# Optimization experiments

Hardware: AMD Instinct MI355X
Metric: run time of the kernel (lower is better)

The kernel has to match this reference:

```python
import jax, jax.numpy as jnp
import numpy as np

EPS = 1e-5  # norm_eps


def setup_inputs() -> dict:
    key = jax.random.key(0)
    ks = jax.random.split(key, 9)
    N, C, T, H, W = 2, 1024, 8, 28, 28
    Di = 512
    s = 0.02  # weight init scale
    return {
        "x": jax.random.normal(ks[0], (N, C, T, H, W), jnp.float32),
        "w_theta": jax.random.normal(ks[1], (Di, C), jnp.float32) * s,
        "b_theta": jax.random.normal(ks[2], (Di,), jnp.float32) * s,
        "w_phi": jax.random.normal(ks[3], (Di, C), jnp.float32) * s,
        "b_phi": jax.random.normal(ks[4], (Di,), jnp.float32) * s,
        "w_g": jax.random.normal(ks[5], (Di, C), jnp.float32) * s,
        "b_g": jax.random.normal(ks[6], (Di,), jnp.float32) * s,
        "w_out": jax.random.normal(ks[7], (C, Di), jnp.float32) * s,
        "b_out": jax.random.normal(ks[8], (C,), jnp.float32) * s,
    }


def reference(x, w_theta, b_theta, w_phi, b_phi, w_g, b_g, w_out, b_out):
    # ProgressNL forward at step==0 (y == x), pool_size=None,
    # instantiation='softmax', norm_type='layernorm' (GroupNorm(1, C, affine=False)).
    N, C, T, H, W = x.shape
    Di = w_theta.shape[0]
    xf = x.reshape(N, C, T * H * W)  # flatten spatio-temporal tokens

    # 1x1x1 convs == per-token matmuls
    theta = jnp.einsum('dc,nct->ndt', w_theta, xf) + b_theta[None, :, None]  # [N,Di,THW]
    phi = jnp.einsum('dc,nct->ndt', w_phi, xf) + b_phi[None, :, None]
    g = jnp.einsum('dc,nct->ndt', w_g, xf) + b_g[None, :, None]

    # attention: softmax(theta^T phi / sqrt(Di)) @ g^T
    scores = jnp.einsum('nct,ncp->ntp', theta, phi) * (Di ** -0.5)  # [N,THW,THW]
    attn = jax.nn.softmax(scores, axis=-1)
    o = jnp.einsum('ntp,ncp->nct', attn, g)  # [N,Di,THW]

    # output 1x1x1 conv
    p = jnp.einsum('cd,ndt->nct', w_out, o) + b_out[None, :, None]  # [N,C,THW]

    # GroupNorm(1, C, affine=False): normalize over (C,T,H,W) per sample
    mean = jnp.mean(p, axis=(1, 2), keepdims=True)
    var = jnp.var(p, axis=(1, 2), keepdims=True)
    p = (p - mean) * jax.lax.rsqrt(var + EPS)

    return x + p.reshape(N, C, T, H, W)
```

## Files before the change

kernel.cpp:

```cpp
#include <hip/hip_runtime.h>

typedef _Float16 f16x8 __attribute__((ext_vector_type(8)));
typedef _Float16 f16x4 __attribute__((ext_vector_type(4)));
typedef float    f32x4 __attribute__((ext_vector_type(4)));

#define THW 6272
#define CCH 1024
#define DI  512

__device__ __forceinline__ void gload16(const _Float16* g, _Float16* l)
{
    __builtin_amdgcn_global_load_lds(
        (const __attribute__((address_space(1))) void*)g,
        (__attribute__((address_space(3))) void*)l, 16, 0, 0);
}

template<typename OUT_T, int BM, bool BIAS_M, bool BIAS_N, bool EXPP>
__global__ __launch_bounds__(256, 3)
void gemm_nt(const _Float16* __restrict__ A, size_t lda, size_t sAn,
             const _Float16* __restrict__ Bt, size_t ldb, size_t sBn,
             OUT_T* __restrict__ C, size_t ldc, size_t sCn,
             int K, float alpha,
             const float* __restrict__ bias_m,
             const float* __restrict__ bias_n,
             float* __restrict__ psum,
             int rows_ps,
             int gx, int gy)
{
    constexpr int MF = BM / 32;
    __shared__ _Float16 As[BM * 64];
    __shared__ _Float16 Bs[128 * 64];
    const int tid  = threadIdx.x;
    const int lane = tid & 63;
    const int wave = tid >> 6;
    const int wr = wave >> 1, wc = wave & 1;

    const int nwg = gridDim.x;
    const int q = nwg >> 3, rr = nwg & 7;
    const int xcd = blockIdx.x & 7, seq = blockIdx.x >> 3;
    const int wg = (xcd < rr ? xcd * (q + 1) : rr * (q + 1) + (xcd - rr) * q) + seq;
    const int zz  = wg / (gx * gy);
    const int rem = wg - zz * gx * gy;
    const int by  = rem / gx, bx = rem - by * gx;
    const int n   = zz & 1;
    const int ks  = zz >> 1;

    A  += (size_t)n * sAn + (size_t)ks * K + (size_t)by * BM * lda;
    Bt += (size_t)n * sBn + (size_t)ks * K + (size_t)bx * 128 * ldb;

    const int srow = lane >> 3, sk = (lane & 7) * 8;
    const _Float16* gA = A  + (size_t)(wave * (MF * 8) + srow) * lda + sk;
    const _Float16* gB = Bt + (size_t)(wave * 32 + srow) * ldb + sk;
    _Float16* lA = As + wave * (MF * 512) + lane * 8;
    _Float16* lB = Bs + wave * 2048 + lane * 8;

    const int r  = lane & 15;
    const int kg = lane >> 4;

    f32x4 acc[MF][4] = {};

    for (int kt = 0; kt < K; kt += 64) {
#pragma unroll
        for (int i = 0; i < MF; i++)
            gload16(gA + (size_t)(i * 8) * lda, lA + i * 512);
#pragma unroll
        for (int i = 0; i < 4; i++)
            gload16(gB + (size_t)(i * 8) * ldb, lB + i * 512);
        gA += 64; gB += 64;
        __syncthreads();
#pragma unroll
        for (int kk = 0; kk < 2; kk++) {
            f16x8 af[MF], bf[4];
#pragma unroll
            for (int mf = 0; mf < MF; mf++)
                af[mf] = *(const f16x8*)(As + (wr * (BM / 2) + mf * 16 + r) * 64 + kk * 32 + kg * 8);
#pragma unroll
            for (int nf = 0; nf < 4; nf++)
                bf[nf] = *(const f16x8*)(Bs + (wc * 64 + nf * 16 + r) * 64 + kk * 32 + kg * 8);
#pragma unroll
            for (int mf = 0; mf < MF; mf++)
#pragma unroll
                for (int nf = 0; nf < 4; nf++)
                    acc[mf][nf] = __builtin_amdgcn_mfma_f32_16x16x32_f16(
                        af[mf], bf[nf], acc[mf][nf], 0, 0, 0);
        }
        __syncthreads();
    }

    C += (size_t)zz * sCn;
#pragma unroll
    for (int mf = 0; mf < MF; mf++) {
#pragma unroll
        for (int qi = 0; qi < 4; qi++) {
            size_t row = (size_t)by * BM + wr * (BM / 2) + mf * 16 + kg * 4 + qi;
            float bm = BIAS_M ? bias_m[row] : 0.f;
            float rsum = 0.f;
#pragma unroll
            for (int nf = 0; nf < 4; nf++) {
                size_t col = (size_t)bx * 128 + wc * 64 + nf * 16 + r;
                float val = acc[mf][nf][qi] * alpha + bm + (BIAS_N ? bias_n[col] : 0.f);
                if (EXPP) {
                    float e = __expf(val);
                    rsum += e;
                    C[row * ldc + col] = (OUT_T)e;
                } else {
                    C[row * ldc + col] = (OUT_T)val;
                }
            }
            if (EXPP) {
                rsum += __shfl_xor(rsum, 1);
                rsum += __shfl_xor(rsum, 2);
                rsum += __shfl_xor(rsum, 4);
                rsum += __shfl_xor(rsum, 8);
                if (r == 0)
                    psum[((size_t)n * rows_ps + row) * 98 + bx * 2 + wc] = rsum;
            }
        }
    }
}

__global__ __launch_bounds__(256)
void rowsum_inv(const float* __restrict__ psum, float* __restrict__ inv, int nrows)
{
    int rI = blockIdx.x * 256 + threadIdx.x;
    if (rI < nrows) {
        const float* p = psum + (size_t)rI * 98;
        float s = 0.f;
#pragma unroll 7
        for (int i = 0; i < 98; i++) s += p[i];
        inv[rI] = 1.f / s;
    }
}

__global__ __launch_bounds__(256)
void combine_scale(const float* __restrict__ Op, const float* __restrict__ inv,
                   _Float16* __restrict__ Ot, int tr, int t0)
{
    const int total4 = tr * 256;
    int idx = blockIdx.x * 256 + threadIdx.x;
    if (idx >= total4) return;
    const int per_n4 = tr * 128;
    int n = idx / per_n4;
    int rem = idx - n * per_n4;
    int t = rem >> 7, d4 = rem & 127;
    const f32x4* p = (const f32x4*)Op;
    f32x4 a = p[(size_t)n * per_n4 + rem];
    f32x4 b = p[(size_t)(2 + n) * per_n4 + rem];
    float sc = inv[(size_t)n * tr + t];
    f16x4 o;
#pragma unroll
    for (int j = 0; j < 4; j++) o[j] = (_Float16)((a[j] + b[j]) * sc);
    *(f16x4*)(Ot + ((size_t)(n * THW + t0 + t) * DI + d4 * 4)) = o;
}

__global__ __launch_bounds__(256)
void pack_weights(const float* __restrict__ wt, const float* __restrict__ wp,
                  const float* __restrict__ wg, const float* __restrict__ wo,
                  const float* __restrict__ bt, const float* __restrict__ bp,
                  _Float16* __restrict__ Wtp, _Float16* __restrict__ Wg,
                  _Float16* __restrict__ Wo, float* __restrict__ btp)
{
    int i = blockIdx.x * 256 + threadIdx.x;
    if (i < 512 * 1024) {
        Wtp[i]              = (_Float16)wt[i];
        Wtp[i + 512 * 1024] = (_Float16)wp[i];
        Wg[i]               = (_Float16)wg[i];
        Wo[i]               = (_Float16)wo[i];
    }
    if (i < 512) { btp[i] = bt[i]; btp[i + 512] = bp[i]; }
}

__global__ __launch_bounds__(256)
void transpose_cast(const float* __restrict__ x, _Float16* __restrict__ xT)
{
    __shared__ float tile[32][33];
    const int n  = blockIdx.z;
    const int t0 = blockIdx.x * 32;
    const int c0 = blockIdx.y * 32;
    const int tx = threadIdx.x & 31, ty = threadIdx.x >> 5;
    const float* xp = x + ((size_t)n * CCH + c0) * THW + t0;
#pragma unroll
    for (int i = 0; i < 4; i++) {
        int c = ty + i * 8;
        tile[c][tx] = xp[(size_t)c * THW + tx];
    }
    __syncthreads();
    _Float16* op = xT + ((size_t)n * THW + t0) * CCH + c0;
#pragma unroll
    for (int i = 0; i < 4; i++) {
        int t = ty + i * 8;
        op[(size_t)t * CCH + tx] = (_Float16)tile[tx][t];
    }
}

__global__ __launch_bounds__(256)
void reduce_partial(const float* __restrict__ pc, float* __restrict__ partials, int nblk)
{
    const size_t per_n4 = (size_t)CCH * THW / 4;
    const int n = blockIdx.y;
    const f32x4* p = (const f32x4*)(pc + (size_t)n * CCH * THW);
    float s = 0.f, s2 = 0.f;
    for (size_t i = (size_t)blockIdx.x * 256 + threadIdx.x; i < per_n4; i += (size_t)nblk * 256) {
        f32x4 xv = p[i];
#pragma unroll
        for (int j = 0; j < 4; j++) { s += xv[j]; s2 += xv[j] * xv[j]; }
    }
    for (int o = 32; o; o >>= 1) { s += __shfl_xor(s, o); s2 += __shfl_xor(s2, o); }
    __shared__ float rs[4], rs2[4];
    if ((threadIdx.x & 63) == 0) { rs[threadIdx.x >> 6] = s; rs2[threadIdx.x >> 6] = s2; }
    __syncthreads();
    if (threadIdx.x == 0) {
        partials[((size_t)n * nblk + blockIdx.x) * 2]     = rs[0] + rs[1] + rs[2] + rs[3];
        partials[((size_t)n * nblk + blockIdx.x) * 2 + 1] = rs2[0] + rs2[1] + rs2[2] + rs2[3];
    }
}

__global__ __launch_bounds__(256)
void reduce_final(const float* __restrict__ partials, float* __restrict__ stats, int nblk)
{
    const int n = blockIdx.x;
    float s = 0.f, s2 = 0.f;
    for (int i = threadIdx.x; i < nblk; i += 256) {
        s  += partials[((size_t)n * nblk + i) * 2];
        s2 += partials[((size_t)n * nblk + i) * 2 + 1];
    }
    for (int o = 32; o; o >>= 1) { s += __shfl_xor(s, o); s2 += __shfl_xor(s2, o); }
    __shared__ float rs[4], rs2[4];
    if ((threadIdx.x & 63) == 0) { rs[threadIdx.x >> 6] = s; rs2[threadIdx.x >> 6] = s2; }
    __syncthreads();
    if (threadIdx.x == 0) {
        float S1 = rs[0] + rs[1] + rs[2] + rs[3];
        float S2 = rs2[0] + rs2[1] + rs2[2] + rs2[3];
        const float invc = 1.f / ((float)CCH * (float)THW);
        float mean = S1 * invc;
        float var  = S2 * invc - mean * mean;
        stats[n * 2]     = mean;
        stats[n * 2 + 1] = rsqrtf(var + 1e-5f);
    }
}

__global__ __launch_bounds__(256)
void final_residual(const float* __restrict__ x, float* __restrict__ pc_out,
                    const float* __restrict__ stats, size_t total4)
{
    const size_t per_n4 = (size_t)CCH * THW / 4;
    for (size_t i = (size_t)blockIdx.x * 256 + threadIdx.x; i < total4;
         i += (size_t)gridDim.x * 256) {
        int n = (int)(i / per_n4);
        float mean = stats[n * 2], rstd = stats[n * 2 + 1];
        f32x4 xv = ((const f32x4*)x)[i];
        f32x4 pv = ((f32x4*)pc_out)[i];
        f32x4 ov;
#pragma unroll
        for (int j = 0; j < 4; j++) ov[j] = xv[j] + (pv[j] - mean) * rstd;
        ((f32x4*)pc_out)[i] = ov;
    }
}

extern "C" void kernel_launch(void* const* d_in, const int* in_sizes, int n_in,
                              void* d_out, int out_size, void* d_ws, size_t ws_size,
                              hipStream_t stream)
{
    const float* x  = (const float*)d_in[0];
    const float* wt = (const float*)d_in[1];
    const float* bt = (const float*)d_in[2];
    const float* wp = (const float*)d_in[3];
    const float* bp = (const float*)d_in[4];
    const float* wg = (const float*)d_in[5];
    const float* bg = (const float*)d_in[6];
    const float* wo = (const float*)d_in[7];
    const float* bo = (const float*)d_in[8];
    float* out = (float*)d_out;

    char* ws = (char*)d_ws;
    size_t off = 0;
    auto alloc = [&](size_t b) -> void* {
        off = (off + 255) & ~(size_t)255;
        void* p = ws + off;
        off += b;
        return p;
    };

    _Float16* Wtp = (_Float16*)alloc((size_t)1024 * 1024 * 2);
    _Float16* Wg  = (_Float16*)alloc((size_t)512 * 1024 * 2);
    _Float16* Wo  = (_Float16*)alloc((size_t)1024 * 512 * 2);
    float*    btp = (float*)alloc(1024 * 4);
    _Float16* xT  = (_Float16*)alloc((size_t)2 * THW * CCH * 2);
    _Float16* tpg = (_Float16*)alloc((size_t)2 * THW * 1024 * 2);
    _Float16* g   = (_Float16*)alloc((size_t)2 * DI * THW * 2);
    _Float16* Ot  = (_Float16*)alloc((size_t)2 * THW * DI * 2);
    float*    partials = (float*)alloc((size_t)2 * 256 * 2 * 4);
    float*    stats    = (float*)alloc(4 * 4);

    const size_t tile_bytes = (size_t)2 * 128 * (THW * 2 + 98 * 4 + 4);
    size_t avail = (ws_size > off + 256) ? ws_size - off - 256 : 0;
    int tiles_fit = (int)(avail / tile_bytes);
    if (tiles_fit < 1) tiles_fit = 1;
    if (tiles_fit > 49) tiles_fit = 49;
    int nch = (49 + tiles_fit - 1) / tiles_fit;
    int tpc = (49 + nch - 1) / nch;

    _Float16* S    = (_Float16*)alloc((size_t)2 * tpc * 128 * THW * 2);
    float*    psum = (float*)alloc((size_t)2 * tpc * 128 * 98 * 4);
    float*    inv  = (float*)alloc((size_t)2 * tpc * 128 * 4);
    float*    Opart = out;

    const size_t sXT = (size_t)THW * CCH;
    const size_t sG  = (size_t)DI * THW;

    pack_weights<<<2048, 256, 0, stream>>>(wt, wp, wg, wo, bt, bp, Wtp, Wg, Wo, btp);
    transpose_cast<<<dim3(THW / 32, CCH / 32, 2), 256, 0, stream>>>(x, xT);

    gemm_nt<_Float16, 128, false, true, false><<<8 * 49 * 2, 256, 0, stream>>>(
        xT, CCH, sXT, Wtp, CCH, 0, tpg, 1024, sXT, CCH, 1.f,
        nullptr, btp, nullptr, 0, 8, 49);

    gemm_nt<_Float16, 64, true, false, false><<<49 * 8 * 2, 256, 0, stream>>>(
        Wg, CCH, 0, xT, CCH, sXT, g, THW, sG, CCH, 1.f,
        bg, nullptr, nullptr, 0, 49, 8);

    const float scale = 0.044194173824159216f;
    for (int ch = 0; ch < nch; ch++) {
        int tile0 = ch * tpc;
        int tiles = (49 - tile0 < tpc) ? (49 - tile0) : tpc;
        size_t t0 = (size_t)tile0 * 128;
        int tchRows = tiles * 128;

        gemm_nt<_Float16, 128, false, false, true><<<49 * tiles * 2, 256, 0, stream>>>(
            tpg + t0 * 1024, 1024, sXT, tpg + 512, 1024, sXT,
            S, THW, (size_t)tchRows * THW, DI, scale,
            nullptr, nullptr, psum, tchRows, 49, tiles);

        rowsum_inv<<<(2 * tchRows + 255) / 256, 256, 0, stream>>>(psum, inv, 2 * tchRows);

        gemm_nt<float, 128, false, false, false><<<4 * tiles * 4, 256, 0, stream>>>(
            S, THW, (size_t)tchRows * THW, g, THW, sG,
            Opart, DI, (size_t)tchRows * DI, THW / 2, 1.f,
            nullptr, nullptr, nullptr, 0, 4, tiles);

        combine_scale<<<(tchRows * 256 + 255) / 256, 256, 0, stream>>>(
            Opart, inv, Ot, tchRows, (int)t0);
    }

    gemm_nt<float, 128, true, false, false><<<49 * 8 * 2, 256, 0, stream>>>(
        Wo, DI, 0, Ot, DI, sG, out, THW, (size_t)CCH * THW, DI, 1.f,
        bo, nullptr, nullptr, 0, 49, 8);

    reduce_partial<<<dim3(256, 2), 256, 0, stream>>>(out, partials, 256);
    reduce_final<<<2, 256, 0, stream>>>(partials, stats, 256);
    final_residual<<<2048, 256, 0, stream>>>(x, out, stats, (size_t)2 * CCH * THW / 4);
}
```

Before: 461.9 us.

## Double-buffer LDS tiles in gemm_nt to overlap global loads with MFMA

Splits the A and B shared-memory tiles into two buffers. The next K-tile is issued with direct global-to-LDS loads before computing on the current one, using a manual vmcnt wait and a raw s_barrier in place of __syncthreads. This hides global load latency behind the MFMA work, but doubles LDS use, so launch bounds drop from 3 to 2 blocks per CU. The hand-counted vmcnt values and the bare barriers could be fragile if the compiler reorders memory operations or the LDS loads need an lgkmcnt wait.

```diff
diff --git a/kernel.cpp b/kernel.cpp
--- a/kernel.cpp
+++ b/kernel.cpp
@@ -16,7 +16,7 @@
 }
 
 template<typename OUT_T, int BM, bool BIAS_M, bool BIAS_N, bool EXPP>
-__global__ __launch_bounds__(256, 3)
+__global__ __launch_bounds__(256, 2)
 void gemm_nt(const _Float16* __restrict__ A, size_t lda, size_t sAn,
              const _Float16* __restrict__ Bt, size_t ldb, size_t sBn,
              OUT_T* __restrict__ C, size_t ldc, size_t sCn,
@@ -28,8 +28,8 @@
              int gx, int gy)
 {
     constexpr int MF = BM / 32;
-    __shared__ _Float16 As[BM * 64];
-    __shared__ _Float16 Bs[128 * 64];
+    __shared__ _Float16 As[2][BM * 64];
+    __shared__ _Float16 Bs[2][128 * 64];
     const int tid  = threadIdx.x;
     const int lane = tid & 63;
     const int wave = tid >> 6;
@@ -51,32 +51,48 @@
     const int srow = lane >> 3, sk = (lane & 7) * 8;
     const _Float16* gA = A  + (size_t)(wave * (MF * 8) + srow) * lda + sk;
     const _Float16* gB = Bt + (size_t)(wave * 32 + srow) * ldb + sk;
-    _Float16* lA = As + wave * (MF * 512) + lane * 8;
-    _Float16* lB = Bs + wave * 2048 + lane * 8;
+    const int lAo = wave * (MF * 512) + lane * 8;
+    const int lBo = wave * 2048 + lane * 8;
 
     const int r  = lane & 15;
     const int kg = lane >> 4;
 
     f32x4 acc[MF][4] = {};
 
-    for (int kt = 0; kt < K; kt += 64) {
+    auto STAGE = [&](int kti, int b) {
+        const _Float16* a  = gA + (size_t)kti * 64;
+        const _Float16* bb = gB + (size_t)kti * 64;
 #pragma unroll
         for (int i = 0; i < MF; i++)
-            gload16(gA + (size_t)(i * 8) * lda, lA + i * 512);
+            gload16(a + (size_t)(i * 8) * lda, &As[b][lAo + i * 512]);
 #pragma unroll
         for (int i = 0; i < 4; i++)
-            gload16(gB + (size_t)(i * 8) * ldb, lB + i * 512);
-        gA += 64; gB += 64;
-        __syncthreads();
+            gload16(bb + (size_t)(i * 8) * ldb, &Bs[b][lBo + i * 512]);
+    };
+
+    const int NT = K >> 6;
+    STAGE(0, 0);
+    for (int t = 0; t < NT; ++t) {
+        const int cur = t & 1;
+        if (t + 1 < NT) {
+            STAGE(t + 1, cur ^ 1);
+            if constexpr (MF == 4)
+                asm volatile("s_waitcnt vmcnt(8)" ::: "memory");
+            else
+                asm volatile("s_waitcnt vmcnt(6)" ::: "memory");
+        } else {
+            asm volatile("s_waitcnt vmcnt(0)" ::: "memory");
+        }
+        __builtin_amdgcn_s_barrier();
 #pragma unroll
         for (int kk = 0; kk < 2; kk++) {
             f16x8 af[MF], bf[4];
 #pragma unroll
             for (int mf = 0; mf < MF; mf++)
-                af[mf] = *(const f16x8*)(As + (wr * (BM / 2) + mf * 16 + r) * 64 + kk * 32 + kg * 8);
+                af[mf] = *(const f16x8*)(&As[cur][(wr * (BM / 2) + mf * 16 + r) * 64 + kk * 32 + kg * 8]);
 #pragma unroll
             for (int nf = 0; nf < 4; nf++)
-                bf[nf] = *(const f16x8*)(Bs + (wc * 64 + nf * 16 + r) * 64 + kk * 32 + kg * 8);
+                bf[nf] = *(const f16x8*)(&Bs[cur][(wc * 64 + nf * 16 + r) * 64 + kk * 32 + kg * 8]);
 #pragma unroll
             for (int mf = 0; mf < MF; mf++)
 #pragma unroll
@@ -84,7 +100,7 @@
                     acc[mf][nf] = __builtin_amdgcn_mfma_f32_16x16x32_f16(
                         af[mf], bf[nf], acc[mf][nf], 0, 0, 0);
         }
-        __syncthreads();
+        __builtin_amdgcn_s_barrier();
     }
 
     C += (size_t)zz * sCn;
```

New measurement: 496.5 us. +7.5%, slower.
